# Kernel tuning notes

Measured on AMD Instinct MI355X. Metric: run time of the kernel, lower is better.

## Reference

```python
import jax, jax.numpy as jnp
import numpy as np

B, T, HID = 2, 2048, 2048
NH = 8
D = HID // NH  # head_dim = 256 (expand_ratio=1 so input_dim == hidden_size)
EPS_RMS = 1e-8   # RMSNorm inside BitLinear
EPS_LN = 1e-5    # layernorm_eps for g_norm


def _rms(x, w, eps):
    # weighted RMSNorm over last dim
    return x * jax.lax.rsqrt(jnp.mean(x * x, axis=-1, keepdims=True) + eps) * w


def _act_quant(x):
    # per-token 8-bit fake quant with straight-through estimator
    s = 127.0 / jnp.clip(jnp.max(jnp.abs(x), axis=-1, keepdims=True), 1e-5)
    q = jnp.clip(jnp.round(x * s), -128, 127) / s
    return x + jax.lax.stop_gradient(q - x)


def _weight_quant(w):
    # ternary weight quantization (BitNet b1.58) with STE
    s = 1.0 / jnp.clip(jnp.mean(jnp.abs(w)), 1e-5)
    q = jnp.clip(jnp.round(w * s), -1, 1) / s
    return w + jax.lax.stop_gradient(q - w)


def _bitlinear(x, w, norm_w):
    # FusedBitLinear: RMSNorm -> activation quant -> ternary-weight linear
    xq = _act_quant(_rms(x, norm_w, EPS_RMS))
    return jnp.einsum('btk,ok->bto', xq, _weight_quant(w))


def setup_inputs() -> dict:
    key = jax.random.key(0)
    ks = jax.random.split(key, 5)
    std = 2 ** (-2.5) * np.sqrt(2.0 / (HID + HID))  # xavier_uniform-ish std with gain 2^-2.5
    return {
        'hidden_states': jax.random.normal(ks[0], (B, T, HID), dtype=jnp.float32),
        'w_i': jax.random.normal(ks[1], (HID, HID), dtype=jnp.float32) * std,
        'w_f': jax.random.normal(ks[2], (HID, HID), dtype=jnp.float32) * std,
        'w_g': jax.random.normal(ks[3], (HID, HID), dtype=jnp.float32) * std,
        'w_o': jax.random.normal(ks[4], (HID, HID), dtype=jnp.float32) * std,
        'n_i': jnp.ones((HID,), jnp.float32),
        'n_f': jnp.ones((HID,), jnp.float32),
        'n_g': jnp.ones((HID,), jnp.float32),
        'n_o': jnp.ones((HID,), jnp.float32),
        'gn_w': jnp.ones((HID,), jnp.float32),
    }


def reference(hidden_states, w_i, w_f, w_g, w_o, n_i, n_f, n_g, n_o, gn_w):
    hs = hidden_states
    i = _bitlinear(hs, w_i, n_i)                      # [B,T,HID]
    f = jax.nn.sigmoid(_bitlinear(hs, w_f, n_f))      # forget gate
    # swiglu(i, 1 - f) = silu(i) * (1 - f)
    i = i * jax.nn.sigmoid(i) * (1.0 - f)

    # b l (h d) -> t b h d for scan
    def to_tbhd(x):
        return x.reshape(B, T, NH, D).transpose(1, 0, 2, 3)

    i_t, f_t = to_tbhd(i), to_tbhd(f)

    def step(h, ft_it):
        ft, it = ft_it
        h = ft * h + it
        return h, h

    h0 = jnp.zeros((B, NH, D), dtype=i.dtype)
    _, o = jax.lax.scan(step, h0, (f_t, i_t))         # [T,B,NH,D]
    o = o.transpose(1, 0, 2, 3).reshape(B, T, HID)     # b l (h d)

    # g_norm(g_proj(hs), o): rmsnorm(g) * o * sigmoid(o)
    g = _bitlinear(hs, w_g, n_g)
    o = _rms(g, gn_w, EPS_LN) * o * jax.nn.sigmoid(o)
    return _bitlinear(o, w_o, n_o)
```

## Files before the change

kernel.cpp:

```cpp
#include <hip/hip_runtime.h>
#include <math.h>

#define HID 2048
#define TOKENS 4096
#define TT 2048
#define NCH 4096
#define NC 32
#define CL 64
#define WELEM 4194304

typedef unsigned short u16;
typedef signed char i8;
typedef int i32x4 __attribute__((ext_vector_type(4)));

__device__ inline float sigm(float x) { return 1.0f / (1.0f + expf(-x)); }

__device__ inline float wred_sum(float v) {
#pragma unroll
  for (int o = 32; o > 0; o >>= 1) v += __shfl_down(v, o);
  return v;
}
__device__ inline float wred_max(float v) {
#pragma unroll
  for (int o = 32; o > 0; o >>= 1) v = fmaxf(v, __shfl_down(v, o));
  return v;
}
__device__ inline double wred_sumd(double v) {
#pragma unroll
  for (int o = 32; o > 0; o >>= 1) v += __shfl_down(v, o);
  return v;
}

__device__ __forceinline__ void gl_lds16(const void* g, void* l) {
  __builtin_amdgcn_global_load_lds(
      (__attribute__((address_space(1))) void*)(void*)g,
      (__attribute__((address_space(3))) void*)l, 16, 0, 0);
}

__device__ __forceinline__ int pack8(const int* qi) {
  return (qi[0] & 255) | ((qi[1] & 255) << 8) | ((qi[2] & 255) << 16)
       | ((qi[3] & 255) << 24);
}

__global__ __launch_bounds__(256) void absmean_kernel(
    const float* __restrict__ w0, const float* __restrict__ w1,
    const float* __restrict__ w2, const float* __restrict__ w3,
    double* __restrict__ wsum) {
  int widx = blockIdx.x >> 9;
  int blk = blockIdx.x & 511;
  const float* w = widx == 0 ? w0 : widx == 1 ? w1 : widx == 2 ? w2 : w3;
  size_t base = (size_t)blk * 8192;
  double acc = 0.0;
#pragma unroll
  for (int r = 0; r < 8; ++r) {
    float4 v = *(const float4*)&w[base + (size_t)(r * 256 + threadIdx.x) * 4];
    acc += (double)fabsf(v.x) + (double)fabsf(v.y) + (double)fabsf(v.z) +
           (double)fabsf(v.w);
  }
  acc = wred_sumd(acc);
  __shared__ double sh[4];
  int tid = threadIdx.x;
  if ((tid & 63) == 0) sh[tid >> 6] = acc;
  __syncthreads();
  if (tid == 0) atomicAdd(&wsum[widx], (sh[0] + sh[1]) + (sh[2] + sh[3]));
}

__global__ __launch_bounds__(256) void wquant4_kernel(
    const float* __restrict__ w0, const float* __restrict__ w1,
    const float* __restrict__ w2, const float* __restrict__ w3,
    const double* __restrict__ wsum, i8* __restrict__ q0, i8* __restrict__ q1,
    i8* __restrict__ q2, i8* __restrict__ q3) {
  int sel = blockIdx.x >> 11;
  int blk = blockIdx.x & 2047;
  const float* w = sel == 0 ? w0 : sel == 1 ? w1 : sel == 2 ? w2 : w3;
  i8* wq = sel == 0 ? q0 : sel == 1 ? q1 : sel == 2 ? q2 : q3;
  int widx = sel == 0 ? 1 : sel == 1 ? 0 : sel;
  double mean = wsum[widx] * (1.0 / (double)WELEM);
  float s = (float)(1.0 / fmax(mean, 1e-5));
  size_t base = (size_t)blk * 2048 + (size_t)threadIdx.x * 8;
  float4 va = *(const float4*)&w[base];
  float4 vb = *(const float4*)&w[base + 4];
  float vv[8] = {va.x, va.y, va.z, va.w, vb.x, vb.y, vb.z, vb.w};
  int qi[8];
#pragma unroll
  for (int j = 0; j < 8; ++j) {
    float q1v = rintf(vv[j] * s);
    q1v = fminf(fmaxf(q1v, -1.0f), 1.0f);
    qi[j] = (int)q1v;
  }
  *(int2*)&wq[base] = make_int2(pack8(qi), pack8(qi + 4));
}

__global__ __launch_bounds__(256) void rmsquant3_kernel(
    const float* __restrict__ X, const float* __restrict__ nw0,
    const float* __restrict__ nw1, const float* __restrict__ nw2,
    i8* __restrict__ Xq0, i8* __restrict__ Xq1, i8* __restrict__ Xq2,
    float* __restrict__ inv0, float* __restrict__ inv1,
    float* __restrict__ inv2) {
  int tok = blockIdx.x;
  int tid = threadIdx.x;
  const float* xrow = X + (size_t)tok * HID;
  int c0 = tid * 8;
  float x[8];
  *(float4*)&x[0] = *(const float4*)&xrow[c0];
  *(float4*)&x[4] = *(const float4*)&xrow[c0 + 4];
  float ss = 0.0f;
#pragma unroll
  for (int j = 0; j < 8; ++j) ss += x[j] * x[j];
  __shared__ float sh[4];
  float v = wred_sum(ss);
  if ((tid & 63) == 0) sh[tid >> 6] = v;
  __syncthreads();
  float tot = (sh[0] + sh[1]) + (sh[2] + sh[3]);
  float rstd = (float)(1.0 / sqrt((double)(tot * (1.0f / HID)) + 1e-8));
#pragma unroll
  for (int pass = 0; pass < 3; ++pass) {
    const float* nw = pass == 0 ? nw0 : pass == 1 ? nw1 : nw2;
    i8* Xq = pass == 0 ? Xq0 : pass == 1 ? Xq1 : Xq2;
    float* inv_s = pass == 0 ? inv0 : pass == 1 ? inv1 : inv2;
    float y[8];
    float amax = 0.0f;
#pragma unroll
    for (int j = 0; j < 8; ++j) {
      y[j] = x[j] * rstd * nw[c0 + j];
      amax = fmaxf(amax, fabsf(y[j]));
    }
    __syncthreads();
    float vv = wred_max(amax);
    if ((tid & 63) == 0) sh[tid >> 6] = vv;
    __syncthreads();
    float am = fmaxf(fmaxf(fmaxf(sh[0], sh[1]), fmaxf(sh[2], sh[3])), 1e-5f);
    float s = 127.0f / am;
    int qi[8];
#pragma unroll
    for (int j = 0; j < 8; ++j) {
      float qq = rintf(y[j] * s);
      qq = fminf(fmaxf(qq, -128.0f), 127.0f);
      qi[j] = (int)qq;
    }
    *(int2*)&Xq[(size_t)tok * HID + c0] = make_int2(pack8(qi), pack8(qi + 4));
    if (tid == 0) inv_s[tok] = am * (1.0f / 127.0f);
  }
}

__global__ __launch_bounds__(512) void gemm8_kernel(
    const i8* __restrict__ Aq, const i8* __restrict__ Wq,
    const float* __restrict__ inv_s, const double* __restrict__ wsum, int widx,
    float* __restrict__ Out, int mode) {
  const int tid = threadIdx.x;
  const int lid = blockIdx.x;
  const int swz = (lid & 7) * 64 + (lid >> 3);
  const int n0 = (swz & 15) * 128;
  const int m0 = (swz >> 4) * 128;

  __shared__ __align__(16) i8 As[2][16384];
  __shared__ __align__(16) i8 Bs[2][16384];
  float wscale = (float)fmax(wsum[widx] * (1.0 / (double)WELEM), 1e-5);

  const int wave = tid >> 6, lane = tid & 63;
  const int wm = wave >> 2;
  const int wn = wave & 3;
  const int lrow = lane & 15;
  const int ksel = lane >> 4;
  const int rsw = lrow & 7;
  const int srow8 = lane >> 3;
  const int scol = ((lane & 7) ^ srow8) << 4;

  const i8* Ab = Aq + (size_t)m0 * HID;
  const i8* Wb = Wq + (size_t)n0 * HID;

  i32x4 acc[4][2];
#pragma unroll
  for (int i = 0; i < 4; ++i)
#pragma unroll
    for (int j = 0; j < 2; ++j)
#pragma unroll
      for (int r = 0; r < 4; ++r) acc[i][j][r] = 0;

#define STAGEH(buf, k0, h)                                                  \
  {                                                                         \
    int chunk = wave * 2 + (h);                                             \
    int row = chunk * 8 + srow8;                                            \
    gl_lds16(&Ab[(size_t)row * HID + (k0) + scol], &As[buf][chunk * 1024]); \
    gl_lds16(&Wb[(size_t)row * HID + (k0) + scol], &Bs[buf][chunk * 1024]); \
  }

#define PHASE(buf, ks)                                                      \
  {                                                                         \
    i32x4 af[4], bfr[2];                                                    \
    _Pragma("unroll") for (int i = 0; i < 4; ++i) {                         \
      int ra = wm * 64 + i * 16 + lrow;                                     \
      int phys = (((ks) << 2) | ksel) ^ rsw;                                \
      af[i] = *(const i32x4*)&As[buf][ra * 128 + phys * 16];                \
    }                                                                       \
    _Pragma("unroll") for (int j = 0; j < 2; ++j) {                         \
      int rb = wn * 32 + j * 16 + lrow;                                     \
      int phys = (((ks) << 2) | ksel) ^ rsw;                                \
      bfr[j] = *(const i32x4*)&Bs[buf][rb * 128 + phys * 16];               \
    }                                                                       \
    __builtin_amdgcn_s_setprio(1);                                          \
    _Pragma("unroll") for (int i = 0; i < 4; ++i)                           \
        _Pragma("unroll") for (int j = 0; j < 2; ++j) acc[i][j] =           \
            __builtin_amdgcn_mfma_i32_16x16x64_i8(af[i], bfr[j], acc[i][j], \
                                                  0, 0, 0);                 \
    __builtin_amdgcn_s_setprio(0);                                          \
  }

  const int NT = HID / 128;
  STAGEH(0, 0, 0)
  STAGEH(0, 0, 1)
  int cur = 0;
  for (int kt = 0; kt < NT; ++kt) {
    asm volatile("s_waitcnt vmcnt(0)" ::: "memory");
    __builtin_amdgcn_s_barrier();
    if (kt + 1 < NT) STAGEH(cur ^ 1, (kt + 1) * 128, 0)
    PHASE(cur, 0)
    __builtin_amdgcn_s_barrier();
    if (kt + 1 < NT) STAGEH(cur ^ 1, (kt + 1) * 128, 1)
    PHASE(cur, 1)
    cur ^= 1;
  }
#undef STAGEH
#undef PHASE

#pragma unroll
  for (int i = 0; i < 4; ++i) {
    int rbase = m0 + wm * 64 + i * 16 + (lane >> 4) * 4;
#pragma unroll
    for (int j = 0; j < 2; ++j) {
      int col = n0 + wn * 32 + j * 16 + lrow;
#pragma unroll
      for (int r = 0; r < 4; ++r) {
        int row = rbase + r;
        float v = (float)acc[i][j][r] * inv_s[row] * wscale;
        size_t oidx = (size_t)row * HID + col;
        if (mode == 0) {
          Out[oidx] = sigm(v);
        } else if (mode == 1) {
          Out[oidx] = v * sigm(v);
        } else {
          Out[oidx] = v;
        }
      }
    }
  }
}

__global__ __launch_bounds__(256) void scan1_kernel(
    const float* __restrict__ F, float* __restrict__ IO, float* __restrict__ P,
    float* __restrict__ H) {
  int c = blockIdx.x * 256 + threadIdx.x;
  int q = blockIdx.y;
  size_t base =
      (size_t)(c >> 11) * TT * HID + (c & 2047) + (size_t)q * CL * HID;
  float h = 0.0f, p = 1.0f;
#pragma unroll 4
  for (int t = 0; t < CL; ++t) {
    size_t idx = base + (size_t)t * HID;
    float f = F[idx];
    float iv = IO[idx];
    h = fmaf(f, h, iv - iv * f);
    p *= f;
    IO[idx] = h;
  }
  P[q * NCH + c] = p;
  H[q * NCH + c] = h;
}

__global__ __launch_bounds__(256) void scan2_kernel(
    const float* __restrict__ P, const float* __restrict__ H,
    float* __restrict__ Ini) {
  int c = blockIdx.x * 256 + threadIdx.x;
  float carry = 0.0f;
#pragma unroll
  for (int q = 0; q < NC; ++q) {
    float pq = P[q * NCH + c];
    float hq = H[q * NCH + c];
    Ini[q * NCH + c] = carry;
    carry = fmaf(pq, carry, hq);
  }
}

__global__ __launch_bounds__(256) void scan3_kernel(
    const float* __restrict__ F, const float* __restrict__ Ini,
    float* __restrict__ IO) {
  int c = blockIdx.x * 256 + threadIdx.x;
  int q = blockIdx.y + 1;
  float h0 = Ini[q * NCH + c];
  if (h0 == 0.0f) return;
  size_t base =
      (size_t)(c >> 11) * TT * HID + (c & 2047) + (size_t)q * CL * HID;
  float p = 1.0f;
#pragma unroll 4
  for (int t = 0; t < CL; ++t) {
    size_t idx = base + (size_t)t * HID;
    p *= F[idx];
    IO[idx] = fmaf(p, h0, IO[idx]);
  }
}

__global__ __launch_bounds__(256) void combine_quant_kernel(
    const float* __restrict__ G, const float* __restrict__ gnw,
    const float* __restrict__ O, const float* __restrict__ nw,
    i8* __restrict__ Xq, float* __restrict__ inv_s) {
  int tok = blockIdx.x;
  int tid = threadIdx.x;
  int c0 = tid * 8;
  const float* grow = G + (size_t)tok * HID;
  const float* orow = O + (size_t)tok * HID;
  float g[8], o[8];
  *(float4*)&g[0] = *(const float4*)&grow[c0];
  *(float4*)&g[4] = *(const float4*)&grow[c0 + 4];
  *(float4*)&o[0] = *(const float4*)&orow[c0];
  *(float4*)&o[4] = *(const float4*)&orow[c0 + 4];
  __shared__ float sh[4];
  float ss = 0.0f;
#pragma unroll
  for (int j = 0; j < 8; ++j) ss += g[j] * g[j];
  float v = wred_sum(ss);
  if ((tid & 63) == 0) sh[tid >> 6] = v;
  __syncthreads();
  float tot = (sh[0] + sh[1]) + (sh[2] + sh[3]);
  float rstd_g = (float)(1.0 / sqrt((double)(tot * (1.0f / HID)) + 1e-5));
  float on[8];
  float ss2 = 0.0f;
#pragma unroll
  for (int j = 0; j < 8; ++j) {
    on[j] = g[j] * rstd_g * gnw[c0 + j] * o[j] * sigm(o[j]);
    ss2 += on[j] * on[j];
  }
  __syncthreads();
  v = wred_sum(ss2);
  if ((tid & 63) == 0) sh[tid >> 6] = v;
  __syncthreads();
  float tot2 = (sh[0] + sh[1]) + (sh[2] + sh[3]);
  float rstd_o = (float)(1.0 / sqrt((double)(tot2 * (1.0f / HID)) + 1e-8));
  float y[8];
  float amax = 0.0f;
#pragma unroll
  for (int j = 0; j < 8; ++j) {
    y[j] = on[j] * rstd_o * nw[c0 + j];
    amax = fmaxf(amax, fabsf(y[j]));
  }
  __syncthreads();
  v = wred_max(amax);
  if ((tid & 63) == 0) sh[tid >> 6] = v;
  __syncthreads();
  float am = fmaxf(fmaxf(fmaxf(sh[0], sh[1]), fmaxf(sh[2], sh[3])), 1e-5f);
  float s = 127.0f / am;
  int qi[8];
#pragma unroll
  for (int j = 0; j < 8; ++j) {
    float qq = rintf(y[j] * s);
    qq = fminf(fmaxf(qq, -128.0f), 127.0f);
    qi[j] = (int)qq;
  }
  *(int2*)&Xq[(size_t)tok * HID + c0] = make_int2(pack8(qi), pack8(qi + 4));
  if (tid == 0) inv_s[tok] = am * (1.0f / 127.0f);
}

extern "C" void kernel_launch(void* const* d_in, const int* in_sizes, int n_in,
                              void* d_out, int out_size, void* d_ws,
                              size_t ws_size, hipStream_t stream) {
  const float* hs = (const float*)d_in[0];
  const float* w_i = (const float*)d_in[1];
  const float* w_f = (const float*)d_in[2];
  const float* w_g = (const float*)d_in[3];
  const float* w_o = (const float*)d_in[4];
  const float* n_i = (const float*)d_in[5];
  const float* n_f = (const float*)d_in[6];
  const float* n_g = (const float*)d_in[7];
  const float* n_o = (const float*)d_in[8];
  const float* gn_w = (const float*)d_in[9];
  float* Out = (float*)d_out;

  char* ws = (char*)d_ws;
  i8* WQ0 = (i8*)ws;
  i8* WQ1 = (i8*)(ws + 4194304);
  i8* WQ2 = (i8*)(ws + 8388608);
  i8* WQ3 = (i8*)(ws + 12582912);
  i8* XQ0 = (i8*)(ws + 16777216);
  i8* XQ1 = (i8*)(ws + 25165824);
  i8* XQ2 = (i8*)(ws + 33554432);
  float* F = (float*)(ws + 41943040);
  float* G = F;
  float* invs0 = (float*)(ws + 75497472);
  float* invs1 = (float*)(ws + 75513856);
  float* invs2 = (float*)(ws + 75530240);
  double* wsum = (double*)(ws + 75546624);
  float* scanP = (float*)(ws + 75547648);
  float* scanH = (float*)(ws + 76071936);

  hipMemsetAsync(wsum, 0, 4 * sizeof(double), stream);
  absmean_kernel<<<2048, 256, 0, stream>>>(w_i, w_f, w_g, w_o, wsum);

  wquant4_kernel<<<8192, 256, 0, stream>>>(w_f, w_i, w_g, w_o, wsum, WQ0, WQ1,
                                           WQ2, WQ3);
  rmsquant3_kernel<<<TOKENS, 256, 0, stream>>>(hs, n_f, n_i, n_g, XQ0, XQ1,
                                               XQ2, invs0, invs1, invs2);

  gemm8_kernel<<<512, 512, 0, stream>>>(XQ0, WQ0, invs0, wsum, 1, F, 0);
  gemm8_kernel<<<512, 512, 0, stream>>>(XQ1, WQ1, invs1, wsum, 0, Out, 1);

  scan1_kernel<<<dim3(NCH / 256, NC), 256, 0, stream>>>(F, Out, scanP, scanH);
  scan2_kernel<<<NCH / 256, 256, 0, stream>>>(scanP, scanH, scanP);
  scan3_kernel<<<dim3(NCH / 256, NC - 1), 256, 0, stream>>>(F, scanP, Out);

  gemm8_kernel<<<512, 512, 0, stream>>>(XQ2, WQ2, invs2, wsum, 2, G, 2);

  combine_quant_kernel<<<TOKENS, 256, 0, stream>>>(G, gn_w, Out, n_o, XQ0,
                                                   invs0);

  gemm8_kernel<<<512, 512, 0, stream>>>(XQ0, WQ3, invs0, wsum, 3, Out, 2);
}
```

Before: 239.7 us.

## Batch three input GEMMs into one launch and store intermediates as bf16

The f, i and g projections now run as one 1536-block launch, with a segment index picking the operands, instead of three separate launches. The F, I/O and G intermediates are stored as bf16 rather than fp32, which halves the memory traffic in the scan and combine kernels. The GEMM main loop is also restructured: the two half-stage phases become one full-tile stage per iteration with a single __syncthreads. The bf16 storage adds rounding error to the recurrence state and gate values, and G now needs its own buffer, which makes the workspace larger.

```diff
diff --git a/kernel.cpp b/kernel.cpp
--- a/kernel.cpp
+++ b/kernel.cpp
@@ -14,6 +14,14 @@
 typedef int i32x4 __attribute__((ext_vector_type(4)));
 
 __device__ inline float sigm(float x) { return 1.0f / (1.0f + expf(-x)); }
+__device__ inline u16 f2bf_rn(float v) {
+  unsigned b = __float_as_uint(v);
+  unsigned r = b + 0x7FFFu + ((b >> 16) & 1u);
+  return (u16)(r >> 16);
+}
+__device__ inline float bf2f(u16 h) {
+  return __uint_as_float((unsigned)h << 16);
+}
 
 __device__ inline float wred_sum(float v) {
 #pragma unroll
@@ -143,15 +151,29 @@
   }
 }
 
+template <int NSEG, bool F32OUT>
 __global__ __launch_bounds__(512) void gemm8_kernel(
-    const i8* __restrict__ Aq, const i8* __restrict__ Wq,
-    const float* __restrict__ inv_s, const double* __restrict__ wsum, int widx,
-    float* __restrict__ Out, int mode) {
+    const i8* __restrict__ A0, const i8* __restrict__ A1,
+    const i8* __restrict__ A2, const i8* __restrict__ W0,
+    const i8* __restrict__ W1, const i8* __restrict__ W2,
+    const float* __restrict__ inv0, const float* __restrict__ inv1,
+    const float* __restrict__ inv2, const double* __restrict__ wsum,
+    int widx0, int widx1, int widx2, void* __restrict__ O0,
+    void* __restrict__ O1, void* __restrict__ O2) {
   const int tid = threadIdx.x;
+  const int cpx = gridDim.x >> 3;
   const int lid = blockIdx.x;
-  const int swz = (lid & 7) * 64 + (lid >> 3);
-  const int n0 = (swz & 15) * 128;
-  const int m0 = (swz >> 4) * 128;
+  const int swz = (lid & 7) * cpx + (lid >> 3);
+  const int seg = NSEG == 1 ? 0 : (swz >> 9);
+  const int idx = swz & 511;
+  const int n0 = (idx & 15) * 128;
+  const int m0 = (idx >> 4) * 128;
+
+  const i8* Aq = seg == 0 ? A0 : seg == 1 ? A1 : A2;
+  const i8* Wq = seg == 0 ? W0 : seg == 1 ? W1 : W2;
+  const float* inv_s = seg == 0 ? inv0 : seg == 1 ? inv1 : inv2;
+  void* Out = seg == 0 ? O0 : seg == 1 ? O1 : O2;
+  const int widx = seg == 0 ? widx0 : seg == 1 ? widx1 : widx2;
 
   __shared__ __align__(16) i8 As[2][16384];
   __shared__ __align__(16) i8 Bs[2][16384];
@@ -177,51 +199,55 @@
 #pragma unroll
       for (int r = 0; r < 4; ++r) acc[i][j][r] = 0;
 
-#define STAGEH(buf, k0, h)                                                  \
+#define STAGE(buf, k0)                                                      \
   {                                                                         \
-    int chunk = wave * 2 + (h);                                             \
-    int row = chunk * 8 + srow8;                                            \
-    gl_lds16(&Ab[(size_t)row * HID + (k0) + scol], &As[buf][chunk * 1024]); \
-    gl_lds16(&Wb[(size_t)row * HID + (k0) + scol], &Bs[buf][chunk * 1024]); \
-  }
-
-#define PHASE(buf, ks)                                                      \
-  {                                                                         \
-    i32x4 af[4], bfr[2];                                                    \
-    _Pragma("unroll") for (int i = 0; i < 4; ++i) {                         \
-      int ra = wm * 64 + i * 16 + lrow;                                     \
-      int phys = (((ks) << 2) | ksel) ^ rsw;                                \
-      af[i] = *(const i32x4*)&As[buf][ra * 128 + phys * 16];                \
+    _Pragma("unroll") for (int c = 0; c < 2; ++c) {                         \
+      int chunk = wave * 2 + c;                                             \
+      int row = chunk * 8 + srow8;                                          \
+      gl_lds16(&Ab[(size_t)row * HID + (k0) + scol], &As[buf][chunk * 1024]); \
+      gl_lds16(&Wb[(size_t)row * HID + (k0) + scol], &Bs[buf][chunk * 1024]); \
     }                                                                       \
-    _Pragma("unroll") for (int j = 0; j < 2; ++j) {                         \
-      int rb = wn * 32 + j * 16 + lrow;                                     \
-      int phys = (((ks) << 2) | ksel) ^ rsw;                                \
-      bfr[j] = *(const i32x4*)&Bs[buf][rb * 128 + phys * 16];               \
-    }                                                                       \
-    __builtin_amdgcn_s_setprio(1);                                          \
-    _Pragma("unroll") for (int i = 0; i < 4; ++i)                           \
-        _Pragma("unroll") for (int j = 0; j < 2; ++j) acc[i][j] =           \
-            __builtin_amdgcn_mfma_i32_16x16x64_i8(af[i], bfr[j], acc[i][j], \
-                                                  0, 0, 0);                 \
-    __builtin_amdgcn_s_setprio(0);                                          \
   }
 
   const int NT = HID / 128;
-  STAGEH(0, 0, 0)
-  STAGEH(0, 0, 1)
+  STAGE(0, 0)
+  __syncthreads();
   int cur = 0;
   for (int kt = 0; kt < NT; ++kt) {
-    asm volatile("s_waitcnt vmcnt(0)" ::: "memory");
-    __builtin_amdgcn_s_barrier();
-    if (kt + 1 < NT) STAGEH(cur ^ 1, (kt + 1) * 128, 0)
-    PHASE(cur, 0)
-    __builtin_amdgcn_s_barrier();
-    if (kt + 1 < NT) STAGEH(cur ^ 1, (kt + 1) * 128, 1)
-    PHASE(cur, 1)
+    if (kt + 1 < NT) STAGE(cur ^ 1, (kt + 1) * 128)
+    i32x4 af[4][2], bfr[2][2];
+#pragma unroll
+    for (int i = 0; i < 4; ++i) {
+      int ra = wm * 64 + i * 16 + lrow;
+#pragma unroll
+      for (int kk = 0; kk < 2; ++kk) {
+        int phys = ((kk << 2) | ksel) ^ rsw;
+        af[i][kk] = *(const i32x4*)&As[cur][ra * 128 + phys * 16];
+      }
+    }
+#pragma unroll
+    for (int j = 0; j < 2; ++j) {
+      int rb = wn * 32 + j * 16 + lrow;
+#pragma unroll
+      for (int kk = 0; kk < 2; ++kk) {
+        int phys = ((kk << 2) | ksel) ^ rsw;
+        bfr[j][kk] = *(const i32x4*)&Bs[cur][rb * 128 + phys * 16];
+      }
+    }
+    __builtin_amdgcn_s_setprio(1);
+#pragma unroll
+    for (int kk = 0; kk < 2; ++kk)
+#pragma unroll
+      for (int i = 0; i < 4; ++i)
+#pragma unroll
+        for (int j = 0; j < 2; ++j)
+          acc[i][j] = __builtin_amdgcn_mfma_i32_16x16x64_i8(
+              af[i][kk], bfr[j][kk], acc[i][j], 0, 0, 0);
+    __builtin_amdgcn_s_setprio(0);
+    __syncthreads();
     cur ^= 1;
   }
-#undef STAGEH
-#undef PHASE
+#undef STAGE
 
 #pragma unroll
   for (int i = 0; i < 4; ++i) {
@@ -233,21 +259,23 @@
       for (int r = 0; r < 4; ++r) {
         int row = rbase + r;
         float v = (float)acc[i][j][r] * inv_s[row] * wscale;
+        float rr;
+        if (NSEG == 3)
+          rr = seg == 0 ? sigm(v) : seg == 1 ? v * sigm(v) : v;
+        else
+          rr = v;
         size_t oidx = (size_t)row * HID + col;
-        if (mode == 0) {
-          Out[oidx] = sigm(v);
-        } else if (mode == 1) {
-          Out[oidx] = v * sigm(v);
-        } else {
-          Out[oidx] = v;
-        }
+        if (F32OUT)
+          ((float*)Out)[oidx] = rr;
+        else
+          ((u16*)Out)[oidx] = f2bf_rn(rr);
       }
     }
   }
 }
 
 __global__ __launch_bounds__(256) void scan1_kernel(
-    const float* __restrict__ F, float* __restrict__ IO, float* __restrict__ P,
+    const u16* __restrict__ F, u16* __restrict__ IO, float* __restrict__ P,
     float* __restrict__ H) {
   int c = blockIdx.x * 256 + threadIdx.x;
   int q = blockIdx.y;
@@ -257,11 +285,11 @@
 #pragma unroll 4
   for (int t = 0; t < CL; ++t) {
     size_t idx = base + (size_t)t * HID;
-    float f = F[idx];
-    float iv = IO[idx];
+    float f = bf2f(F[idx]);
+    float iv = bf2f(IO[idx]);
     h = fmaf(f, h, iv - iv * f);
     p *= f;
-    IO[idx] = h;
+    IO[idx] = f2bf_rn(h);
   }
   P[q * NCH + c] = p;
   H[q * NCH + c] = h;
@@ -282,8 +310,8 @@
 }
 
 __global__ __launch_bounds__(256) void scan3_kernel(
-    const float* __restrict__ F, const float* __restrict__ Ini,
-    float* __restrict__ IO) {
+    const u16* __restrict__ F, const float* __restrict__ Ini,
+    u16* __restrict__ IO) {
   int c = blockIdx.x * 256 + threadIdx.x;
   int q = blockIdx.y + 1;
   float h0 = Ini[q * NCH + c];
@@ -294,25 +322,28 @@
 #pragma unroll 4
   for (int t = 0; t < CL; ++t) {
     size_t idx = base + (size_t)t * HID;
-    p *= F[idx];
-    IO[idx] = fmaf(p, h0, IO[idx]);
+    p *= bf2f(F[idx]);
+    IO[idx] = f2bf_rn(fmaf(p, h0, bf2f(IO[idx])));
   }
 }
 
 __global__ __launch_bounds__(256) void combine_quant_kernel(
-    const float* __restrict__ G, const float* __restrict__ gnw,
-    const float* __restrict__ O, const float* __restrict__ nw,
+    const u16* __restrict__ G, const float* __restrict__ gnw,
+    const u16* __restrict__ O, const float* __restrict__ nw,
     i8* __restrict__ Xq, float* __restrict__ inv_s) {
   int tok = blockIdx.x;
   int tid = threadIdx.x;
   int c0 = tid * 8;
-  const float* grow = G + (size_t)tok * HID;
-  const float* orow = O + (size_t)tok * HID;
-  float g[8], o[8];
-  *(float4*)&g[0] = *(const float4*)&grow[c0];
-  *(float4*)&g[4] = *(const float4*)&grow[c0 + 4];
-  *(float4*)&o[0] = *(const float4*)&orow[c0];
-  *(float4*)&o[4] = *(const float4*)&orow[c0 + 4];
+  const u16* grow = G + (size_t)tok * HID;
+  const u16* orow = O + (size_t)tok * HID;
+  ushort4 ga = *(const ushort4*)&grow[c0];
+  ushort4 gb = *(const ushort4*)&grow[c0 + 4];
+  ushort4 oa = *(const ushort4*)&orow[c0];
+  ushort4 ob = *(const ushort4*)&orow[c0 + 4];
+  float g[8] = {bf2f(ga.x), bf2f(ga.y), bf2f(ga.z), bf2f(ga.w),
+                bf2f(gb.x), bf2f(gb.y), bf2f(gb.z), bf2f(gb.w)};
+  float o[8] = {bf2f(oa.x), bf2f(oa.y), bf2f(oa.z), bf2f(oa.w),
+                bf2f(ob.x), bf2f(ob.y), bf2f(ob.z), bf2f(ob.w)};
   __shared__ float sh[4];
   float ss = 0.0f;
 #pragma unroll
@@ -382,14 +413,15 @@
   i8* XQ0 = (i8*)(ws + 16777216);
   i8* XQ1 = (i8*)(ws + 25165824);
   i8* XQ2 = (i8*)(ws + 33554432);
-  float* F = (float*)(ws + 41943040);
-  float* G = F;
-  float* invs0 = (float*)(ws + 75497472);
-  float* invs1 = (float*)(ws + 75513856);
-  float* invs2 = (float*)(ws + 75530240);
-  double* wsum = (double*)(ws + 75546624);
-  float* scanP = (float*)(ws + 75547648);
-  float* scanH = (float*)(ws + 76071936);
+  u16* F = (u16*)(ws + 41943040);
+  u16* OB = (u16*)(ws + 58720256);
+  u16* G = (u16*)(ws + 75497472);
+  float* invs0 = (float*)(ws + 92274688);
+  float* invs1 = (float*)(ws + 92291072);
+  float* invs2 = (float*)(ws + 92307456);
+  double* wsum = (double*)(ws + 92323840);
+  float* scanP = (float*)(ws + 92324864);
+  float* scanH = (float*)(ws + 92849152);
 
   hipMemsetAsync(wsum, 0, 4 * sizeof(double), stream);
   absmean_kernel<<<2048, 256, 0, stream>>>(w_i, w_f, w_g, w_o, wsum);
@@ -399,17 +431,18 @@
   rmsquant3_kernel<<<TOKENS, 256, 0, stream>>>(hs, n_f, n_i, n_g, XQ0, XQ1,
                                                XQ2, invs0, invs1, invs2);
 
-  gemm8_kernel<<<512, 512, 0, stream>>>(XQ0, WQ0, invs0, wsum, 1, F, 0);
-  gemm8_kernel<<<512, 512, 0, stream>>>(XQ1, WQ1, invs1, wsum, 0, Out, 1);
-
-  scan1_kernel<<<dim3(NCH / 256, NC), 256, 0, stream>>>(F, Out, scanP, scanH);
+  gemm8_kernel<3, false><<<1536, 512, 0, stream>>>(
+      XQ0, XQ1, XQ2, WQ0, WQ1, WQ2, invs0, invs1, invs2, wsum, 1, 0, 2, F, OB,
+      G);
+
+  scan1_kernel<<<dim3(NCH / 256, NC), 256, 0, stream>>>(F, OB, scanP, scanH);
   scan2_kernel<<<NCH / 256, 256, 0, stream>>>(scanP, scanH, scanP);
-  scan3_kernel<<<dim3(NCH / 256, NC - 1), 256, 0, stream>>>(F, scanP, Out);
-
-  gemm8_kernel<<<512, 512, 0, stream>>>(XQ2, WQ2, invs2, wsum, 2, G, 2);
-
-  combine_quant_kernel<<<TOKENS, 256, 0, stream>>>(G, gn_w, Out, n_o, XQ0,
+  scan3_kernel<<<dim3(NCH / 256, NC - 1), 256, 0, stream>>>(F, scanP, OB);
+
+  combine_quant_kernel<<<TOKENS, 256, 0, stream>>>(G, gn_w, OB, n_o, XQ0,
                                                    invs0);
 
-  gemm8_kernel<<<512, 512, 0, stream>>>(XQ0, WQ3, invs0, wsum, 3, Out, 2);
-}
+  gemm8_kernel<1, true><<<512, 512, 0, stream>>>(
+      XQ0, XQ0, XQ0, WQ3, WQ3, WQ3, invs0, invs0, invs0, wsum, 3, 3, 3, Out,
+      Out, Out);
+}
```

After: 200.9 us. -16.2%, faster.
